# Kernel tuning notes

Measured on AMD Instinct MI355X. Metric: run time of the kernel, lower is better.

The kernel has to match this reference:

```python
import jax, jax.numpy as jnp
import numpy as np

N_NODES = 50000
N_EDGES = 1000000
IN_DIM = 64
HID_DIM = 64
OUT_DIM = 8
N_GRAPHS = 64


def _glorot(key, shape):
    fan_in, fan_out = shape[0], shape[1]
    lim = float(np.sqrt(6.0 / (fan_in + fan_out)))
    return jax.random.uniform(key, shape, jnp.float32, -lim, lim)


def setup_inputs() -> dict:
    key = jax.random.key(0)
    ks = jax.random.split(key, 10)
    x = jax.random.normal(ks[0], (N_NODES, IN_DIM), jnp.float32)
    edge_index = jax.random.randint(ks[1], (2, N_EDGES), 0, N_NODES, jnp.int64)
    batch = jnp.sort(jax.random.randint(ks[2], (N_NODES,), 0, N_GRAPHS, jnp.int64))
    return {
        "x": x,
        "edge_index": edge_index,
        "batch": batch,
        # SAGEConv1: lin_l (applied to aggregated neighbors, has bias), lin_r (root)
        "W1_l": _glorot(ks[3], (IN_DIM, HID_DIM)),
        "b1": jnp.zeros((HID_DIM,), jnp.float32),
        "W1_r": _glorot(ks[4], (IN_DIM, HID_DIM)),
        # SAGEConv2
        "W2_l": _glorot(ks[5], (HID_DIM, HID_DIM)),
        "b2": jnp.zeros((HID_DIM,), jnp.float32),
        "W2_r": _glorot(ks[6], (HID_DIM, HID_DIM)),
        # final Linear
        "W_fc": _glorot(ks[7], (HID_DIM, OUT_DIM)),
        "b_fc": jnp.zeros((OUT_DIM,), jnp.float32),
    }


def _sage_conv(x, src, dst, W_l, b, W_r):
    # PyG SAGEConv (mean aggr): out = lin_l(mean_{j in N(i)} x_j) + lin_r(x_i)
    msg_sum = jax.ops.segment_sum(x[src], dst, num_segments=N_NODES)  # [N, d]
    deg = jax.ops.segment_sum(jnp.ones((src.shape[0],), x.dtype), dst,
                              num_segments=N_NODES)
    mean = msg_sum / jnp.maximum(deg, 1.0)[:, None]
    return mean @ W_l + b + x @ W_r


def reference(x, edge_index, batch, W1_l, b1, W1_r, W2_l, b2, W2_r, W_fc, b_fc):
    src, dst = edge_index[0], edge_index[1]
    h = jax.nn.relu(_sage_conv(x, src, dst, W1_l, b1, W1_r))
    h = jax.nn.relu(_sage_conv(h, src, dst, W2_l, b2, W2_r))
    # global_mean_pool over graph ids
    pooled_sum = jax.ops.segment_sum(h, batch, num_segments=N_GRAPHS)  # [G, d]
    counts = jax.ops.segment_sum(jnp.ones((N_NODES,), h.dtype), batch,
                                 num_segments=N_GRAPHS)
    pooled = pooled_sum / jnp.maximum(counts, 1.0)[:, None]
    return pooled @ W_fc + b_fc
```

## Files before the change

### kernel.cpp

```cpp
#include <hip/hip_runtime.h>
#include <hip/hip_bf16.h>

#define N_NODES 50000
#define N_EDGES 1000000
#define DIM 64
#define N_GRAPHS 64
#define OUT_DIM 8
#define NBLK_SCAN 196
#define NPART 8
#define SUBBLK 16
#define NODES_PER_PART (N_NODES / NPART)
#define NB_RP 512
#define CHUNK_E4 489
#define B_STRIDE 8192
#define POOL_NPW 64
#define LMPAD 80

typedef __attribute__((ext_vector_type(8))) short short8;
typedef __attribute__((ext_vector_type(4))) float f32x4;
typedef __attribute__((ext_vector_type(4))) int v4i;

__device__ __forceinline__ unsigned short f2b(float f) {
    __hip_bfloat16 h = __float2bfloat16(f);
    return *reinterpret_cast<unsigned short*>(&h);
}
__device__ __forceinline__ float b2f(unsigned short u) {
    __hip_bfloat16 h = *reinterpret_cast<__hip_bfloat16*>(&u);
    return __bfloat162float(h);
}

__global__ void histB_kernel(const int* __restrict__ dst, int* __restrict__ blockcnt) {
    __shared__ int sc[NPART];
    if (threadIdx.x < NPART) sc[threadIdx.x] = 0;
    __syncthreads();

    int e4lo = blockIdx.x * CHUNK_E4;
    int e4hi = e4lo + CHUNK_E4; if (e4hi > N_EDGES / 4) e4hi = N_EDGES / 4;

    int c0 = 0, c1 = 0, c2 = 0, c3 = 0, c4 = 0, c5 = 0, c6 = 0, c7 = 0;
    for (int e4 = e4lo + threadIdx.x; e4 < e4hi; e4 += 256) {
        v4i d = ((const v4i*)dst)[e4];
#define CNT1(DD)                                                              \
        {                                                                     \
            unsigned p = (unsigned)(DD) / NODES_PER_PART;                     \
            c0 += (p == 0); c1 += (p == 1); c2 += (p == 2); c3 += (p == 3);   \
            c4 += (p == 4); c5 += (p == 5); c6 += (p == 6); c7 += (p == 7);   \
        }
        CNT1(d.x) CNT1(d.y) CNT1(d.z) CNT1(d.w)
#undef CNT1
    }
    #pragma unroll
    for (int off = 32; off > 0; off >>= 1) {
        c0 += __shfl_xor(c0, off); c1 += __shfl_xor(c1, off);
        c2 += __shfl_xor(c2, off); c3 += __shfl_xor(c3, off);
        c4 += __shfl_xor(c4, off); c5 += __shfl_xor(c5, off);
        c6 += __shfl_xor(c6, off); c7 += __shfl_xor(c7, off);
    }
    if ((threadIdx.x & 63) == 0) {
        atomicAdd(&sc[0], c0); atomicAdd(&sc[1], c1);
        atomicAdd(&sc[2], c2); atomicAdd(&sc[3], c3);
        atomicAdd(&sc[4], c4); atomicAdd(&sc[5], c5);
        atomicAdd(&sc[6], c6); atomicAdd(&sc[7], c7);
    }
    __syncthreads();
    if (threadIdx.x < NPART) blockcnt[blockIdx.x * NPART + threadIdx.x] = sc[threadIdx.x];
}

__global__ void scan8_kernel(const int* __restrict__ blockcnt,
                             int* __restrict__ abs_off, int* __restrict__ bucket_base) {
    __shared__ int part[1024];
    int t = threadIdx.x;
    int v[4], s = 0;
    #pragma unroll
    for (int i = 0; i < 4; ++i) {
        int e = 4 * t + i;
        int p = e >> 9, b = e & (NB_RP - 1);
        v[i] = blockcnt[b * NPART + p];
        s += v[i];
    }
    part[t] = s;
    __syncthreads();
    for (int off = 1; off < 1024; off <<= 1) {
        int u = (t >= off) ? part[t - off] : 0;
        __syncthreads();
        part[t] += u;
        __syncthreads();
    }
    int base = (t == 0) ? 0 : part[t - 1];
    #pragma unroll
    for (int i = 0; i < 4; ++i) {
        int e = 4 * t + i;
        abs_off[e] = base;
        if (i == 0 && (t & 127) == 0) bucket_base[t >> 7] = base;
        base += v[i];
    }
    if (t == 1023) bucket_base[NPART] = N_EDGES;
}

__global__ void scatterP_kernel(const int* __restrict__ src, const int* __restrict__ dst,
                                const int* __restrict__ abs_off,
                                int* __restrict__ db, int* __restrict__ sb) {
    __shared__ int lcur[NPART];
    if (threadIdx.x < NPART)
        lcur[threadIdx.x] = abs_off[threadIdx.x * NB_RP + blockIdx.x];
    __syncthreads();

    int e4lo = blockIdx.x * CHUNK_E4;
    int e4hi = e4lo + CHUNK_E4; if (e4hi > N_EDGES / 4) e4hi = N_EDGES / 4;

    for (int e4 = e4lo + threadIdx.x; e4 < e4hi; e4 += 256) {
        v4i d = ((const v4i*)dst)[e4];
        v4i s = ((const v4i*)src)[e4];
#define PUT1(DD, SS)                                                          \
        {                                                                     \
            unsigned p = (unsigned)(DD) / NODES_PER_PART;                     \
            int pos = atomicAdd(&lcur[p], 1);                                 \
            db[pos] = (DD); sb[pos] = (SS);                                   \
        }
        PUT1(d.x, s.x) PUT1(d.y, s.y) PUT1(d.z, s.z) PUT1(d.w, s.w)
#undef PUT1
    }
}

__global__ void count_priv_kernel(const int* __restrict__ db,
                                  const int* __restrict__ bucket_base,
                                  int* __restrict__ privhist) {
    __shared__ int lh[NODES_PER_PART];
    int p = blockIdx.x & (NPART - 1);
    int sub = blockIdx.x >> 3;
    for (int i = threadIdx.x; i < NODES_PER_PART; i += 256) lh[i] = 0;
    __syncthreads();

    int lo = bucket_base[p], hi = bucket_base[p + 1];
    int len = hi - lo;
    int chunk = (len + SUBBLK - 1) / SUBBLK;
    int clo = lo + sub * chunk;
    int chi = clo + chunk; if (chi > hi) chi = hi;
    int nbase = p * NODES_PER_PART;

    for (int i = clo + threadIdx.x; i < chi; i += 256)
        atomicAdd(&lh[db[i] - nbase], 1);
    __syncthreads();

    int* o = privhist + (size_t)blockIdx.x * NODES_PER_PART;
    for (int i = threadIdx.x; i < NODES_PER_PART; i += 256) o[i] = lh[i];
}

__global__ void merge_hist_kernel(int* __restrict__ privhist, int* __restrict__ cnt,
                                  int* __restrict__ bsum) {
    __shared__ int sd[256];
    int t = threadIdx.x;
    int n = blockIdx.x * 256 + t;
    int run = 0;
    if (n < N_NODES) {
        int p = n / NODES_PER_PART;
        int nl = n - p * NODES_PER_PART;
        #pragma unroll
        for (int b = 0; b < SUBBLK; ++b) {
            size_t idx = (size_t)(b * NPART + p) * NODES_PER_PART + nl;
            int v = privhist[idx];
            privhist[idx] = run;
            run += v;
        }
        cnt[n] = run;
    }
    sd[t] = (n < N_NODES) ? run : 0;
    __syncthreads();
    for (int off = 128; off > 0; off >>= 1) {
        if (t < off) sd[t] += sd[t + off];
        __syncthreads();
    }
    if (t == 0) bsum[blockIdx.x] = sd[0];
}

__global__ void scan_bsum_kernel(const int* __restrict__ bsum, int* __restrict__ boff,
                                 int* __restrict__ row_start) {
    __shared__ int sd[256];
    int t = threadIdx.x;
    int v = (t < NBLK_SCAN) ? bsum[t] : 0;
    sd[t] = v;
    __syncthreads();
    for (int off = 1; off < 256; off <<= 1) {
        int u = (t >= off) ? sd[t - off] : 0;
        __syncthreads();
        sd[t] += u;
        __syncthreads();
    }
    if (t < NBLK_SCAN) boff[t] = sd[t] - v;
    if (t == 0) row_start[N_NODES] = N_EDGES;
}

__global__ void scan_write_kernel(const int* __restrict__ cnt, const int* __restrict__ boff,
                                  int* __restrict__ row_start) {
    __shared__ int sd[256];
    int t = threadIdx.x;
    int idx = blockIdx.x * 256 + t;
    int v = (idx < N_NODES) ? cnt[idx] : 0;
    sd[t] = v;
    __syncthreads();
    for (int off = 1; off < 256; off <<= 1) {
        int u = (t >= off) ? sd[t - off] : 0;
        __syncthreads();
        sd[t] += u;
        __syncthreads();
    }
    if (idx < N_NODES) row_start[idx] = sd[t] - v + boff[blockIdx.x];
}

__global__ void fill_det_kernel(const int* __restrict__ db, const int* __restrict__ sb,
                                const int* __restrict__ bucket_base,
                                const int* __restrict__ row_start,
                                const int* __restrict__ privhist,
                                int* __restrict__ csr) {
    __shared__ int cur[NODES_PER_PART];
    int p = blockIdx.x & (NPART - 1);
    int sub = blockIdx.x >> 3;
    int nbase = p * NODES_PER_PART;
    const int* ph = privhist + (size_t)blockIdx.x * NODES_PER_PART;
    for (int i = threadIdx.x; i < NODES_PER_PART; i += 256)
        cur[i] = row_start[nbase + i] + ph[i];
    __syncthreads();

    int lo = bucket_base[p], hi = bucket_base[p + 1];
    int len = hi - lo;
    int chunk = (len + SUBBLK - 1) / SUBBLK;
    int clo = lo + sub * chunk;
    int chi = clo + chunk; if (chi > hi) chi = hi;

    for (int i = clo + threadIdx.x; i < chi; i += 256) {
        int d = db[i];
        int s = sb[i];
        int pos = atomicAdd(&cur[d - nbase], 1);
        csr[pos] = s;
    }
}

__global__ void xcvt_kernel(const float* __restrict__ x, unsigned short* __restrict__ xb) {
    int i = blockIdx.x * 256 + threadIdx.x;
    if (i >= N_NODES * DIM / 4) return;
    float4 v = ((const float4*)x)[i];
    ushort4 u;
    u.x = f2b(v.x); u.y = f2b(v.y); u.z = f2b(v.z); u.w = f2b(v.w);
    ((ushort4*)xb)[i] = u;
}

__global__ void prep_b_kernel(const float* __restrict__ W1l, const float* __restrict__ W1r,
                              const float* __restrict__ W2l, const float* __restrict__ W2r,
                              unsigned short* __restrict__ Bf) {
    int t = blockIdx.x * 256 + threadIdx.x;
    if (t >= 2048) return;
    int layer = t >> 10;
    int rem = t & 1023;
    int ks = rem >> 8;
    int nt = (rem >> 6) & 3;
    int lane = rem & 63;
    int gq = lane >> 4;
    int col = nt * 16 + (lane & 15);
    const float* Wl = layer ? W2l : W1l;
    const float* Wr = layer ? W2r : W1r;
    unsigned short* o = Bf + (size_t)layer * B_STRIDE + ((ks * 4 + nt) * 64 + lane) * 8;
    #pragma unroll
    for (int i = 0; i < 8; ++i) {
        int k = ks * 32 + gq * 8 + i;
        float v = (k < DIM) ? Wl[k * DIM + col] : Wr[(k - DIM) * DIM + col];
        o[i] = f2b(v);
    }
}

__global__ __launch_bounds__(256) void sage_fused_kernel(
        const unsigned short* __restrict__ feat,
        const int* __restrict__ row_start,
        const int* __restrict__ csr,
        const unsigned short* __restrict__ Bf,
        const float* __restrict__ bias,
        unsigned short* __restrict__ outb) {
    __shared__ unsigned short lmean[16][LMPAD];
    int n0 = blockIdx.x * 16;
    int wid = threadIdx.x >> 6;
    int lane = threadIdx.x & 63;
    int grp = lane >> 4;
    int fi = lane & 15;

    for (int rr = 0; rr < 4; ++rr) {
        int n = n0 + 4 * wid + rr;
        int rs = row_start[n], re = row_start[n + 1];

        float4 a0 = make_float4(0.f, 0.f, 0.f, 0.f);
        float4 a1 = make_float4(0.f, 0.f, 0.f, 0.f);
        int i = rs;
        for (; i + 8 <= re; i += 8) {
            int s0 = csr[i + grp];
            int s1 = csr[i + 4 + grp];
            ushort4 u0 = ((const ushort4*)(feat + (size_t)s0 * DIM))[fi];
            ushort4 u1 = ((const ushort4*)(feat + (size_t)s1 * DIM))[fi];
            a0.x += b2f(u0.x); a0.y += b2f(u0.y); a0.z += b2f(u0.z); a0.w += b2f(u0.w);
            a1.x += b2f(u1.x); a1.y += b2f(u1.y); a1.z += b2f(u1.z); a1.w += b2f(u1.w);
        }
        if (i + 4 <= re) {
            int s = csr[i + grp];
            ushort4 u = ((const ushort4*)(feat + (size_t)s * DIM))[fi];
            a0.x += b2f(u.x); a0.y += b2f(u.y); a0.z += b2f(u.z); a0.w += b2f(u.w);
            i += 4;
        }
        if (i + grp < re) {
            int s = csr[i + grp];
            ushort4 u = ((const ushort4*)(feat + (size_t)s * DIM))[fi];
            a1.x += b2f(u.x); a1.y += b2f(u.y); a1.z += b2f(u.z); a1.w += b2f(u.w);
        }
        float4 acc = make_float4(a0.x + a1.x, a0.y + a1.y, a0.z + a1.z, a0.w + a1.w);

        acc.x += __shfl_xor(acc.x, 16); acc.y += __shfl_xor(acc.y, 16);
        acc.z += __shfl_xor(acc.z, 16); acc.w += __shfl_xor(acc.w, 16);
        acc.x += __shfl_xor(acc.x, 32); acc.y += __shfl_xor(acc.y, 32);
        acc.z += __shfl_xor(acc.z, 32); acc.w += __shfl_xor(acc.w, 32);

        if (grp == 0) {
            float inv = 1.0f / fmaxf((float)(re - rs), 1.0f);
            ushort4 m;
            m.x = f2b(acc.x * inv); m.y = f2b(acc.y * inv);
            m.z = f2b(acc.z * inv); m.w = f2b(acc.w * inv);
            ((ushort4*)&lmean[4 * wid + rr][0])[fi] = m;
        }
    }
    __syncthreads();

    const short8* Bv = (const short8*)Bf;
    short8 bk0 = Bv[(0 * 4 + wid) * 64 + lane];
    short8 bk1 = Bv[(1 * 4 + wid) * 64 + lane];
    short8 bk2 = Bv[(2 * 4 + wid) * 64 + lane];
    short8 bk3 = Bv[(3 * 4 + wid) * 64 + lane];

    int g = lane >> 4;
    int r = lane & 15;
    f32x4 acc = {0.f, 0.f, 0.f, 0.f};

    short8 a;
    a = *(const short8*)&lmean[r][g * 8];
    acc = __builtin_amdgcn_mfma_f32_16x16x32_bf16(a, bk0, acc, 0, 0, 0);
    a = *(const short8*)&lmean[r][32 + g * 8];
    acc = __builtin_amdgcn_mfma_f32_16x16x32_bf16(a, bk1, acc, 0, 0, 0);
    const unsigned short* axp = feat + (size_t)(n0 + r) * DIM + g * 8;
    a = *(const short8*)(axp);
    acc = __builtin_amdgcn_mfma_f32_16x16x32_bf16(a, bk2, acc, 0, 0, 0);
    a = *(const short8*)(axp + 32);
    acc = __builtin_amdgcn_mfma_f32_16x16x32_bf16(a, bk3, acc, 0, 0, 0);

    float bc = bias[wid * 16 + r];
    #pragma unroll
    for (int i = 0; i < 4; ++i) {
        float v = fmaxf(acc[i] + bc, 0.0f);
        outb[(size_t)(n0 + 4 * g + i) * DIM + wid * 16 + r] = f2b(v);
    }
}

__global__ void pool_b_kernel(const unsigned short* __restrict__ h,
                              const int* __restrict__ batch,
                              float* __restrict__ psum, float* __restrict__ pcnt) {
    int wv = (blockIdx.x * blockDim.x + threadIdx.x) >> 6;
    int start = wv * POOL_NPW;
    if (start >= N_NODES) return;
    int j = threadIdx.x & 63;
    int end = start + POOL_NPW;
    if (end > N_NODES) end = N_NODES;

    int g = batch[start];
    float acc = 0.0f, cnt = 0.0f;
    for (int n = start; n < end; ++n) {
        int gn = batch[n];
        if (gn != g) {
            atomicAdd(&psum[g * DIM + j], acc);
            if (j == 0) atomicAdd(&pcnt[g], cnt);
            g = gn; acc = 0.0f; cnt = 0.0f;
        }
        acc += b2f(h[(size_t)n * DIM + j]);
        cnt += 1.0f;
    }
    atomicAdd(&psum[g * DIM + j], acc);
    if (j == 0) atomicAdd(&pcnt[g], cnt);
}

__global__ void fc_kernel(const float* __restrict__ psum,
                          const float* __restrict__ pcnt,
                          const float* __restrict__ Wfc,
                          const float* __restrict__ bfc,
                          float* __restrict__ out) {
    int tid = threadIdx.x;
    if (tid >= N_GRAPHS * OUT_DIM) return;
    int g = tid >> 3;
    int o = tid & 7;
    float inv = 1.0f / fmaxf(pcnt[g], 1.0f);
    float s = bfc[o];
    #pragma unroll
    for (int k = 0; k < DIM; ++k) {
        s += psum[g * DIM + k] * inv * Wfc[k * OUT_DIM + o];
    }
    out[g * OUT_DIM + o] = s;
}

extern "C" void kernel_launch(void* const* d_in, const int* in_sizes, int n_in,
                              void* d_out, int out_size, void* d_ws, size_t ws_size,
                              hipStream_t stream) {
    const float* x   = (const float*)d_in[0];
    const int* ei    = (const int*)d_in[1];
    const int* batch = (const int*)d_in[2];
    const float* W1l = (const float*)d_in[3];
    const float* b1  = (const float*)d_in[4];
    const float* W1r = (const float*)d_in[5];
    const float* W2l = (const float*)d_in[6];
    const float* b2  = (const float*)d_in[7];
    const float* W2r = (const float*)d_in[8];
    const float* Wfc = (const float*)d_in[9];
    const float* bfc = (const float*)d_in[10];
    float* out = (float*)d_out;

    const int* src = ei;
    const int* dst = ei + N_EDGES;

    const size_t SZ_BF   = (size_t)N_NODES * DIM * 2;
    const size_t SZ_CSR  = (size_t)N_EDGES * sizeof(int);
    const size_t SZ_CNT  = ((size_t)(N_NODES + 1) * sizeof(int) + 255) & ~(size_t)255;
    char* ws = (char*)d_ws;
    int*   csr       = (int*)(ws);
    int*   cnt       = (int*)(ws + SZ_CSR);
    int*   row_start = (int*)(ws + SZ_CSR + SZ_CNT);
    char*  tail      = ws + SZ_CSR + 2 * SZ_CNT;
    int*   bsum      = (int*)(tail);
    int*   boff      = bsum + 256;
    int*   blockcnt  = boff + 256;
    int*   abs_off   = blockcnt + NB_RP * NPART;
    int*   bucket_base = abs_off + NB_RP * NPART;
    unsigned short* Bf = (unsigned short*)(bucket_base + 16);
    float* psum      = (float*)((char*)Bf + 2 * B_STRIDE * 2);
    float* pcnt      = psum + N_GRAPHS * DIM;
    char*  regionA   = (char*)(pcnt + N_GRAPHS) + 4096;
    regionA = (char*)(((size_t)regionA + 255) & ~(size_t)255);
    int*   db        = (int*)(regionA);
    int*   sb        = (int*)(regionA + SZ_CSR);
    int*   privhist  = (int*)(regionA + 2 * SZ_CSR);
    unsigned short* xb    = (unsigned short*)(regionA);
    unsigned short* h1b   = (unsigned short*)(regionA + SZ_BF);
    unsigned short* h2b   = (unsigned short*)(regionA + 2 * SZ_BF);

    const int fusedBlocks = N_NODES / 16;
    const int xcvtBlocks  = (N_NODES * DIM / 4 + 255) / 256;
    const int poolWaves   = (N_NODES + POOL_NPW - 1) / POOL_NPW;
    const int poolBlocks  = (poolWaves + 3) / 4;

    hipMemsetAsync(psum, 0, (size_t)(N_GRAPHS * DIM + N_GRAPHS) * sizeof(float), stream);

    histB_kernel<<<NB_RP, 256, 0, stream>>>(dst, blockcnt);
    scan8_kernel<<<1, 1024, 0, stream>>>(blockcnt, abs_off, bucket_base);
    scatterP_kernel<<<NB_RP, 256, 0, stream>>>(src, dst, abs_off, db, sb);
    count_priv_kernel<<<NPART * SUBBLK, 256, 0, stream>>>(db, bucket_base, privhist);
    merge_hist_kernel<<<NBLK_SCAN, 256, 0, stream>>>(privhist, cnt, bsum);
    scan_bsum_kernel<<<1, 256, 0, stream>>>(bsum, boff, row_start);
    scan_write_kernel<<<NBLK_SCAN, 256, 0, stream>>>(cnt, boff, row_start);
    fill_det_kernel<<<NPART * SUBBLK, 256, 0, stream>>>(db, sb, bucket_base, row_start,
                                                        privhist, csr);

    xcvt_kernel<<<xcvtBlocks, 256, 0, stream>>>(x, xb);
    prep_b_kernel<<<8, 256, 0, stream>>>(W1l, W1r, W2l, W2r, Bf);

    sage_fused_kernel<<<fusedBlocks, 256, 0, stream>>>(xb, row_start, csr, Bf, b1, h1b);
    sage_fused_kernel<<<fusedBlocks, 256, 0, stream>>>(h1b, row_start, csr,
                                                       Bf + B_STRIDE, b2, h2b);
    pool_b_kernel<<<poolBlocks, 256, 0, stream>>>(h2b, batch, psum, pcnt);
    fc_kernel<<<1, 512, 0, stream>>>(psum, pcnt, Wfc, bfc, out);
}
```

Measured before the change: 160.7 us.

## Fuse CSR build, weight prep and x conversion into one cooperative kernel

Replaces the memset and ten separate preprocessing launches (histogram, scans, scatter, private counts, merge, row_start scan, fill, x conversion, weight packing) with a single cooperative kernel of 512 blocks that uses grid-wide syncs between phases. The intent is to remove per-launch overhead and inter-kernel gaps. The x conversion is folded into the first phase and overlaps the histogram, so xb/h1b/h2b are moved to a separate region no longer aliased with db/sb/privhist. In exchange it adds grid.sync barriers and a block-level rescan of bsum in every scan block, and it requires all 512 blocks to be co-resident.

```diff
diff --git a/kernel.cpp b/kernel.cpp
--- a/kernel.cpp
+++ b/kernel.cpp
@@ -1,5 +1,8 @@
 #include <hip/hip_runtime.h>
 #include <hip/hip_bf16.h>
+#include <hip/hip_cooperative_groups.h>
+
+namespace cg = cooperative_groups;
 
 #define N_NODES 50000
 #define N_EDGES 1000000
@@ -29,241 +32,233 @@
     return __bfloat162float(h);
 }
 
-__global__ void histB_kernel(const int* __restrict__ dst, int* __restrict__ blockcnt) {
-    __shared__ int sc[NPART];
-    if (threadIdx.x < NPART) sc[threadIdx.x] = 0;
-    __syncthreads();
-
-    int e4lo = blockIdx.x * CHUNK_E4;
-    int e4hi = e4lo + CHUNK_E4; if (e4hi > N_EDGES / 4) e4hi = N_EDGES / 4;
-
-    int c0 = 0, c1 = 0, c2 = 0, c3 = 0, c4 = 0, c5 = 0, c6 = 0, c7 = 0;
-    for (int e4 = e4lo + threadIdx.x; e4 < e4hi; e4 += 256) {
-        v4i d = ((const v4i*)dst)[e4];
+struct BuildArgs {
+    const float* x; unsigned short* xb;
+    const float* W1l; const float* W1r; const float* W2l; const float* W2r;
+    unsigned short* Bf;
+    const int* src; const int* dst;
+    int* blockcnt; int* abs_off; int* bucket_base;
+    int* db; int* sb; int* privhist; int* cnt; int* bsum; int* row_start; int* csr;
+    float* psum;
+};
+
+__global__ __launch_bounds__(256) void build_kernel(BuildArgs a) {
+    cg::grid_group grid = cg::this_grid();
+    __shared__ int smem[NODES_PER_PART];
+    const int tid = threadIdx.x;
+    const int bid = blockIdx.x;
+
+    if (bid == 0) {
+        for (int i = tid; i < N_GRAPHS * DIM + N_GRAPHS; i += 256) a.psum[i] = 0.0f;
+    }
+    if (bid == 1) {
+        for (int t = tid; t < 2048; t += 256) {
+            int layer = t >> 10;
+            int rem = t & 1023;
+            int ks = rem >> 8;
+            int nt = (rem >> 6) & 3;
+            int lane = rem & 63;
+            int gq = lane >> 4;
+            int col = nt * 16 + (lane & 15);
+            const float* Wl = layer ? a.W2l : a.W1l;
+            const float* Wr = layer ? a.W2r : a.W1r;
+            unsigned short* o = a.Bf + (size_t)layer * B_STRIDE + ((ks * 4 + nt) * 64 + lane) * 8;
+            #pragma unroll
+            for (int i = 0; i < 8; ++i) {
+                int k = ks * 32 + gq * 8 + i;
+                float v = (k < DIM) ? Wl[k * DIM + col] : Wr[(k - DIM) * DIM + col];
+                o[i] = f2b(v);
+            }
+        }
+    }
+    for (int i = bid * 256 + tid; i < N_NODES * DIM / 4; i += NB_RP * 256) {
+        float4 v = ((const float4*)a.x)[i];
+        ushort4 u;
+        u.x = f2b(v.x); u.y = f2b(v.y); u.z = f2b(v.z); u.w = f2b(v.w);
+        ((ushort4*)a.xb)[i] = u;
+    }
+    {
+        int* sc = smem;
+        if (tid < NPART) sc[tid] = 0;
+        __syncthreads();
+        int e4lo = bid * CHUNK_E4;
+        int e4hi = e4lo + CHUNK_E4; if (e4hi > N_EDGES / 4) e4hi = N_EDGES / 4;
+        int c0 = 0, c1 = 0, c2 = 0, c3 = 0, c4 = 0, c5 = 0, c6 = 0, c7 = 0;
+        for (int e4 = e4lo + tid; e4 < e4hi; e4 += 256) {
+            v4i d = ((const v4i*)a.dst)[e4];
 #define CNT1(DD)                                                              \
-        {                                                                     \
-            unsigned p = (unsigned)(DD) / NODES_PER_PART;                     \
-            c0 += (p == 0); c1 += (p == 1); c2 += (p == 2); c3 += (p == 3);   \
-            c4 += (p == 4); c5 += (p == 5); c6 += (p == 6); c7 += (p == 7);   \
-        }
-        CNT1(d.x) CNT1(d.y) CNT1(d.z) CNT1(d.w)
+            {                                                                 \
+                unsigned p = (unsigned)(DD) / NODES_PER_PART;                 \
+                c0 += (p == 0); c1 += (p == 1); c2 += (p == 2); c3 += (p == 3); \
+                c4 += (p == 4); c5 += (p == 5); c6 += (p == 6); c7 += (p == 7); \
+            }
+            CNT1(d.x) CNT1(d.y) CNT1(d.z) CNT1(d.w)
 #undef CNT1
-    }
-    #pragma unroll
-    for (int off = 32; off > 0; off >>= 1) {
-        c0 += __shfl_xor(c0, off); c1 += __shfl_xor(c1, off);
-        c2 += __shfl_xor(c2, off); c3 += __shfl_xor(c3, off);
-        c4 += __shfl_xor(c4, off); c5 += __shfl_xor(c5, off);
-        c6 += __shfl_xor(c6, off); c7 += __shfl_xor(c7, off);
-    }
-    if ((threadIdx.x & 63) == 0) {
-        atomicAdd(&sc[0], c0); atomicAdd(&sc[1], c1);
-        atomicAdd(&sc[2], c2); atomicAdd(&sc[3], c3);
-        atomicAdd(&sc[4], c4); atomicAdd(&sc[5], c5);
-        atomicAdd(&sc[6], c6); atomicAdd(&sc[7], c7);
-    }
-    __syncthreads();
-    if (threadIdx.x < NPART) blockcnt[blockIdx.x * NPART + threadIdx.x] = sc[threadIdx.x];
-}
-
-__global__ void scan8_kernel(const int* __restrict__ blockcnt,
-                             int* __restrict__ abs_off, int* __restrict__ bucket_base) {
-    __shared__ int part[1024];
-    int t = threadIdx.x;
-    int v[4], s = 0;
-    #pragma unroll
-    for (int i = 0; i < 4; ++i) {
-        int e = 4 * t + i;
-        int p = e >> 9, b = e & (NB_RP - 1);
-        v[i] = blockcnt[b * NPART + p];
-        s += v[i];
-    }
-    part[t] = s;
-    __syncthreads();
-    for (int off = 1; off < 1024; off <<= 1) {
-        int u = (t >= off) ? part[t - off] : 0;
-        __syncthreads();
-        part[t] += u;
-        __syncthreads();
-    }
-    int base = (t == 0) ? 0 : part[t - 1];
-    #pragma unroll
-    for (int i = 0; i < 4; ++i) {
-        int e = 4 * t + i;
-        abs_off[e] = base;
-        if (i == 0 && (t & 127) == 0) bucket_base[t >> 7] = base;
-        base += v[i];
-    }
-    if (t == 1023) bucket_base[NPART] = N_EDGES;
-}
-
-__global__ void scatterP_kernel(const int* __restrict__ src, const int* __restrict__ dst,
-                                const int* __restrict__ abs_off,
-                                int* __restrict__ db, int* __restrict__ sb) {
-    __shared__ int lcur[NPART];
-    if (threadIdx.x < NPART)
-        lcur[threadIdx.x] = abs_off[threadIdx.x * NB_RP + blockIdx.x];
-    __syncthreads();
-
-    int e4lo = blockIdx.x * CHUNK_E4;
-    int e4hi = e4lo + CHUNK_E4; if (e4hi > N_EDGES / 4) e4hi = N_EDGES / 4;
-
-    for (int e4 = e4lo + threadIdx.x; e4 < e4hi; e4 += 256) {
-        v4i d = ((const v4i*)dst)[e4];
-        v4i s = ((const v4i*)src)[e4];
+        }
+        #pragma unroll
+        for (int off = 32; off > 0; off >>= 1) {
+            c0 += __shfl_xor(c0, off); c1 += __shfl_xor(c1, off);
+            c2 += __shfl_xor(c2, off); c3 += __shfl_xor(c3, off);
+            c4 += __shfl_xor(c4, off); c5 += __shfl_xor(c5, off);
+            c6 += __shfl_xor(c6, off); c7 += __shfl_xor(c7, off);
+        }
+        if ((tid & 63) == 0) {
+            atomicAdd(&sc[0], c0); atomicAdd(&sc[1], c1);
+            atomicAdd(&sc[2], c2); atomicAdd(&sc[3], c3);
+            atomicAdd(&sc[4], c4); atomicAdd(&sc[5], c5);
+            atomicAdd(&sc[6], c6); atomicAdd(&sc[7], c7);
+        }
+        __syncthreads();
+        if (tid < NPART) a.blockcnt[bid * NPART + tid] = sc[tid];
+    }
+    grid.sync();
+
+    if (bid == 0) {
+        int* part = smem;
+        int v[16], s = 0;
+        #pragma unroll
+        for (int i = 0; i < 16; ++i) {
+            int e = 16 * tid + i;
+            int p = e >> 9, b = e & (NB_RP - 1);
+            v[i] = a.blockcnt[b * NPART + p];
+            s += v[i];
+        }
+        part[tid] = s;
+        __syncthreads();
+        for (int off = 1; off < 256; off <<= 1) {
+            int u = (tid >= off) ? part[tid - off] : 0;
+            __syncthreads();
+            part[tid] += u;
+            __syncthreads();
+        }
+        int base = (tid == 0) ? 0 : part[tid - 1];
+        #pragma unroll
+        for (int i = 0; i < 16; ++i) {
+            int e = 16 * tid + i;
+            a.abs_off[e] = base;
+            if ((e & (NB_RP - 1)) == 0) a.bucket_base[e >> 9] = base;
+            base += v[i];
+        }
+        if (tid == 0) a.bucket_base[NPART] = N_EDGES;
+    }
+    grid.sync();
+
+    {
+        int* lcur = smem;
+        if (tid < NPART) lcur[tid] = a.abs_off[tid * NB_RP + bid];
+        __syncthreads();
+        int e4lo = bid * CHUNK_E4;
+        int e4hi = e4lo + CHUNK_E4; if (e4hi > N_EDGES / 4) e4hi = N_EDGES / 4;
+        for (int e4 = e4lo + tid; e4 < e4hi; e4 += 256) {
+            v4i d = ((const v4i*)a.dst)[e4];
+            v4i s = ((const v4i*)a.src)[e4];
 #define PUT1(DD, SS)                                                          \
-        {                                                                     \
-            unsigned p = (unsigned)(DD) / NODES_PER_PART;                     \
-            int pos = atomicAdd(&lcur[p], 1);                                 \
-            db[pos] = (DD); sb[pos] = (SS);                                   \
-        }
-        PUT1(d.x, s.x) PUT1(d.y, s.y) PUT1(d.z, s.z) PUT1(d.w, s.w)
+            {                                                                 \
+                unsigned p = (unsigned)(DD) / NODES_PER_PART;                 \
+                int pos = atomicAdd(&lcur[p], 1);                             \
+                a.db[pos] = (DD); a.sb[pos] = (SS);                           \
+            }
+            PUT1(d.x, s.x) PUT1(d.y, s.y) PUT1(d.z, s.z) PUT1(d.w, s.w)
 #undef PUT1
-    }
-}
-
-__global__ void count_priv_kernel(const int* __restrict__ db,
-                                  const int* __restrict__ bucket_base,
-                                  int* __restrict__ privhist) {
-    __shared__ int lh[NODES_PER_PART];
-    int p = blockIdx.x & (NPART - 1);
-    int sub = blockIdx.x >> 3;
-    for (int i = threadIdx.x; i < NODES_PER_PART; i += 256) lh[i] = 0;
-    __syncthreads();
-
-    int lo = bucket_base[p], hi = bucket_base[p + 1];
-    int len = hi - lo;
-    int chunk = (len + SUBBLK - 1) / SUBBLK;
-    int clo = lo + sub * chunk;
-    int chi = clo + chunk; if (chi > hi) chi = hi;
-    int nbase = p * NODES_PER_PART;
-
-    for (int i = clo + threadIdx.x; i < chi; i += 256)
-        atomicAdd(&lh[db[i] - nbase], 1);
-    __syncthreads();
-
-    int* o = privhist + (size_t)blockIdx.x * NODES_PER_PART;
-    for (int i = threadIdx.x; i < NODES_PER_PART; i += 256) o[i] = lh[i];
-}
-
-__global__ void merge_hist_kernel(int* __restrict__ privhist, int* __restrict__ cnt,
-                                  int* __restrict__ bsum) {
-    __shared__ int sd[256];
-    int t = threadIdx.x;
-    int n = blockIdx.x * 256 + t;
-    int run = 0;
-    if (n < N_NODES) {
-        int p = n / NODES_PER_PART;
-        int nl = n - p * NODES_PER_PART;
-        #pragma unroll
-        for (int b = 0; b < SUBBLK; ++b) {
-            size_t idx = (size_t)(b * NPART + p) * NODES_PER_PART + nl;
-            int v = privhist[idx];
-            privhist[idx] = run;
-            run += v;
-        }
-        cnt[n] = run;
-    }
-    sd[t] = (n < N_NODES) ? run : 0;
-    __syncthreads();
-    for (int off = 128; off > 0; off >>= 1) {
-        if (t < off) sd[t] += sd[t + off];
-        __syncthreads();
-    }
-    if (t == 0) bsum[blockIdx.x] = sd[0];
-}
-
-__global__ void scan_bsum_kernel(const int* __restrict__ bsum, int* __restrict__ boff,
-                                 int* __restrict__ row_start) {
-    __shared__ int sd[256];
-    int t = threadIdx.x;
-    int v = (t < NBLK_SCAN) ? bsum[t] : 0;
-    sd[t] = v;
-    __syncthreads();
-    for (int off = 1; off < 256; off <<= 1) {
-        int u = (t >= off) ? sd[t - off] : 0;
-        __syncthreads();
-        sd[t] += u;
-        __syncthreads();
-    }
-    if (t < NBLK_SCAN) boff[t] = sd[t] - v;
-    if (t == 0) row_start[N_NODES] = N_EDGES;
-}
-
-__global__ void scan_write_kernel(const int* __restrict__ cnt, const int* __restrict__ boff,
-                                  int* __restrict__ row_start) {
-    __shared__ int sd[256];
-    int t = threadIdx.x;
-    int idx = blockIdx.x * 256 + t;
-    int v = (idx < N_NODES) ? cnt[idx] : 0;
-    sd[t] = v;
-    __syncthreads();
-    for (int off = 1; off < 256; off <<= 1) {
-        int u = (t >= off) ? sd[t - off] : 0;
-        __syncthreads();
-        sd[t] += u;
-        __syncthreads();
-    }
-    if (idx < N_NODES) row_start[idx] = sd[t] - v + boff[blockIdx.x];
-}
-
-__global__ void fill_det_kernel(const int* __restrict__ db, const int* __restrict__ sb,
-                                const int* __restrict__ bucket_base,
-                                const int* __restrict__ row_start,
-                                const int* __restrict__ privhist,
-                                int* __restrict__ csr) {
-    __shared__ int cur[NODES_PER_PART];
-    int p = blockIdx.x & (NPART - 1);
-    int sub = blockIdx.x >> 3;
-    int nbase = p * NODES_PER_PART;
-    const int* ph = privhist + (size_t)blockIdx.x * NODES_PER_PART;
-    for (int i = threadIdx.x; i < NODES_PER_PART; i += 256)
-        cur[i] = row_start[nbase + i] + ph[i];
-    __syncthreads();
-
-    int lo = bucket_base[p], hi = bucket_base[p + 1];
-    int len = hi - lo;
-    int chunk = (len + SUBBLK - 1) / SUBBLK;
-    int clo = lo + sub * chunk;
-    int chi = clo + chunk; if (chi > hi) chi = hi;
-
-    for (int i = clo + threadIdx.x; i < chi; i += 256) {
-        int d = db[i];
-        int s = sb[i];
-        int pos = atomicAdd(&cur[d - nbase], 1);
-        csr[pos] = s;
-    }
-}
-
-__global__ void xcvt_kernel(const float* __restrict__ x, unsigned short* __restrict__ xb) {
-    int i = blockIdx.x * 256 + threadIdx.x;
-    if (i >= N_NODES * DIM / 4) return;
-    float4 v = ((const float4*)x)[i];
-    ushort4 u;
-    u.x = f2b(v.x); u.y = f2b(v.y); u.z = f2b(v.z); u.w = f2b(v.w);
-    ((ushort4*)xb)[i] = u;
-}
-
-__global__ void prep_b_kernel(const float* __restrict__ W1l, const float* __restrict__ W1r,
-                              const float* __restrict__ W2l, const float* __restrict__ W2r,
-                              unsigned short* __restrict__ Bf) {
-    int t = blockIdx.x * 256 + threadIdx.x;
-    if (t >= 2048) return;
-    int layer = t >> 10;
-    int rem = t & 1023;
-    int ks = rem >> 8;
-    int nt = (rem >> 6) & 3;
-    int lane = rem & 63;
-    int gq = lane >> 4;
-    int col = nt * 16 + (lane & 15);
-    const float* Wl = layer ? W2l : W1l;
-    const float* Wr = layer ? W2r : W1r;
-    unsigned short* o = Bf + (size_t)layer * B_STRIDE + ((ks * 4 + nt) * 64 + lane) * 8;
-    #pragma unroll
-    for (int i = 0; i < 8; ++i) {
-        int k = ks * 32 + gq * 8 + i;
-        float v = (k < DIM) ? Wl[k * DIM + col] : Wr[(k - DIM) * DIM + col];
-        o[i] = f2b(v);
+        }
+    }
+    grid.sync();
+
+    if (bid < NPART * SUBBLK) {
+        int* lh = smem;
+        int p = bid & (NPART - 1);
+        int sub = bid >> 3;
+        for (int i = tid; i < NODES_PER_PART; i += 256) lh[i] = 0;
+        __syncthreads();
+        int lo = a.bucket_base[p], hi = a.bucket_base[p + 1];
+        int len = hi - lo;
+        int chunk = (len + SUBBLK - 1) / SUBBLK;
+        int clo = lo + sub * chunk;
+        int chi = clo + chunk; if (chi > hi) chi = hi;
+        int nbase = p * NODES_PER_PART;
+        for (int i = clo + tid; i < chi; i += 256)
+            atomicAdd(&lh[a.db[i] - nbase], 1);
+        __syncthreads();
+        int* o = a.privhist + (size_t)bid * NODES_PER_PART;
+        for (int i = tid; i < NODES_PER_PART; i += 256) o[i] = lh[i];
+    }
+    grid.sync();
+
+    if (bid < NBLK_SCAN) {
+        int* sd = smem;
+        int n = bid * 256 + tid;
+        int run = 0;
+        if (n < N_NODES) {
+            int p = n / NODES_PER_PART;
+            int nl = n - p * NODES_PER_PART;
+            #pragma unroll
+            for (int b = 0; b < SUBBLK; ++b) {
+                size_t idx = (size_t)(b * NPART + p) * NODES_PER_PART + nl;
+                int v = a.privhist[idx];
+                a.privhist[idx] = run;
+                run += v;
+            }
+            a.cnt[n] = run;
+        }
+        sd[tid] = (n < N_NODES) ? run : 0;
+        __syncthreads();
+        for (int off = 128; off > 0; off >>= 1) {
+            if (tid < off) sd[tid] += sd[tid + off];
+            __syncthreads();
+        }
+        if (tid == 0) a.bsum[bid] = sd[0];
+    }
+    grid.sync();
+
+    if (bid < NBLK_SCAN) {
+        int* sb_ = smem;
+        int* sd2 = smem + 256;
+        int* pboffs = smem + 512;
+        int v = (tid < NBLK_SCAN) ? a.bsum[tid] : 0;
+        sb_[tid] = v;
+        __syncthreads();
+        for (int off = 1; off < 256; off <<= 1) {
+            int u = (tid >= off) ? sb_[tid - off] : 0;
+            __syncthreads();
+            sb_[tid] += u;
+            __syncthreads();
+        }
+        if (tid == 0) *pboffs = sb_[bid] - a.bsum[bid];
+        int idx = bid * 256 + tid;
+        int c = (idx < N_NODES) ? a.cnt[idx] : 0;
+        sd2[tid] = c;
+        __syncthreads();
+        for (int off = 1; off < 256; off <<= 1) {
+            int u = (tid >= off) ? sd2[tid - off] : 0;
+            __syncthreads();
+            sd2[tid] += u;
+            __syncthreads();
+        }
+        if (idx < N_NODES) a.row_start[idx] = sd2[tid] - c + *pboffs;
+        if (bid == 0 && tid == 0) a.row_start[N_NODES] = N_EDGES;
+    }
+    grid.sync();
+
+    if (bid < NPART * SUBBLK) {
+        int* cur = smem;
+        int p = bid & (NPART - 1);
+        int sub = bid >> 3;
+        int nbase = p * NODES_PER_PART;
+        const int* ph = a.privhist + (size_t)bid * NODES_PER_PART;
+        for (int i = tid; i < NODES_PER_PART; i += 256)
+            cur[i] = a.row_start[nbase + i] + ph[i];
+        __syncthreads();
+        int lo = a.bucket_base[p], hi = a.bucket_base[p + 1];
+        int len = hi - lo;
+        int chunk = (len + SUBBLK - 1) / SUBBLK;
+        int clo = lo + sub * chunk;
+        int chi = clo + chunk; if (chi > hi) chi = hi;
+        for (int i = clo + tid; i < chi; i += 256) {
+            int d = a.db[i];
+            int s = a.sb[i];
+            int pos = atomicAdd(&cur[d - nbase], 1);
+            a.csr[pos] = s;
+        }
     }
 }
 
@@ -334,16 +329,16 @@
     int r = lane & 15;
     f32x4 acc = {0.f, 0.f, 0.f, 0.f};
 
-    short8 a;
-    a = *(const short8*)&lmean[r][g * 8];
-    acc = __builtin_amdgcn_mfma_f32_16x16x32_bf16(a, bk0, acc, 0, 0, 0);
-    a = *(const short8*)&lmean[r][32 + g * 8];
-    acc = __builtin_amdgcn_mfma_f32_16x16x32_bf16(a, bk1, acc, 0, 0, 0);
+    short8 aa;
+    aa = *(const short8*)&lmean[r][g * 8];
+    acc = __builtin_amdgcn_mfma_f32_16x16x32_bf16(aa, bk0, acc, 0, 0, 0);
+    aa = *(const short8*)&lmean[r][32 + g * 8];
+    acc = __builtin_amdgcn_mfma_f32_16x16x32_bf16(aa, bk1, acc, 0, 0, 0);
     const unsigned short* axp = feat + (size_t)(n0 + r) * DIM + g * 8;
-    a = *(const short8*)(axp);
-    acc = __builtin_amdgcn_mfma_f32_16x16x32_bf16(a, bk2, acc, 0, 0, 0);
-    a = *(const short8*)(axp + 32);
-    acc = __builtin_amdgcn_mfma_f32_16x16x32_bf16(a, bk3, acc, 0, 0, 0);
+    aa = *(const short8*)(axp);
+    acc = __builtin_amdgcn_mfma_f32_16x16x32_bf16(aa, bk2, acc, 0, 0, 0);
+    aa = *(const short8*)(axp + 32);
+    acc = __builtin_amdgcn_mfma_f32_16x16x32_bf16(aa, bk3, acc, 0, 0, 0);
 
     float bc = bias[wid * 16 + r];
     #pragma unroll
@@ -442,24 +437,24 @@
     unsigned short* h2b   = (unsigned short*)(regionA + 2 * SZ_BF);
 
     const int fusedBlocks = N_NODES / 16;
-    const int xcvtBlocks  = (N_NODES * DIM / 4 + 255) / 256;
     const int poolWaves   = (N_NODES + POOL_NPW - 1) / POOL_NPW;
     const int poolBlocks  = (poolWaves + 3) / 4;
 
-    hipMemsetAsync(psum, 0, (size_t)(N_GRAPHS * DIM + N_GRAPHS) * sizeof(float), stream);
-
-    histB_kernel<<<NB_RP, 256, 0, stream>>>(dst, blockcnt);
-    scan8_kernel<<<1, 1024, 0, stream>>>(blockcnt, abs_off, bucket_base);
-    scatterP_kernel<<<NB_RP, 256, 0, stream>>>(src, dst, abs_off, db, sb);
-    count_priv_kernel<<<NPART * SUBBLK, 256, 0, stream>>>(db, bucket_base, privhist);
-    merge_hist_kernel<<<NBLK_SCAN, 256, 0, stream>>>(privhist, cnt, bsum);
-    scan_bsum_kernel<<<1, 256, 0, stream>>>(bsum, boff, row_start);
-    scan_write_kernel<<<NBLK_SCAN, 256, 0, stream>>>(cnt, boff, row_start);
-    fill_det_kernel<<<NPART * SUBBLK, 256, 0, stream>>>(db, sb, bucket_base, row_start,
-                                                        privhist, csr);
-
-    xcvt_kernel<<<xcvtBlocks, 256, 0, stream>>>(x, xb);
-    prep_b_kernel<<<8, 256, 0, stream>>>(W1l, W1r, W2l, W2r, Bf);
+    xb  = (unsigned short*)(regionA + 2 * SZ_CSR + (size_t)NPART * SUBBLK * NODES_PER_PART * sizeof(int));
+    h1b = xb + N_NODES * DIM;
+    h2b = h1b + N_NODES * DIM;
+
+    BuildArgs ba;
+    ba.x = x; ba.xb = xb;
+    ba.W1l = W1l; ba.W1r = W1r; ba.W2l = W2l; ba.W2r = W2r; ba.Bf = Bf;
+    ba.src = src; ba.dst = dst;
+    ba.blockcnt = blockcnt; ba.abs_off = abs_off; ba.bucket_base = bucket_base;
+    ba.db = db; ba.sb = sb; ba.privhist = privhist; ba.cnt = cnt; ba.bsum = bsum;
+    ba.row_start = row_start; ba.csr = csr; ba.psum = psum;
+
+    void* kargs[] = { &ba };
+    hipLaunchCooperativeKernel((const void*)build_kernel, dim3(NB_RP), dim3(256),
+                               kargs, 0, stream);
 
     sage_fused_kernel<<<fusedBlocks, 256, 0, stream>>>(xb, row_start, csr, Bf, b1, h1b);
     sage_fused_kernel<<<fusedBlocks, 256, 0, stream>>>(h1b, row_start, csr,
```

Measured after the change: 468.5 us. 191% more time.
